# Optimization experiments

Hardware: AMD Instinct MI355X
Metric: run time of the kernel (lower is better)

## Reference

```python
import jax, jax.numpy as jnp
import numpy as np

N_NODES = 50000
N_EDGES = 800000
N_GRAPHS = 256
IN_DIM = 128
HID = 512            # hidden_layer_size
H2 = HID // 2        # 256, conv channels
H4 = HID // 4        # 128


def _linear_init(key, fan_in, fan_out):
    kw, kb = jax.random.split(key)
    bound = 1.0 / np.sqrt(fan_in)
    W = jax.random.uniform(kw, (fan_in, fan_out), minval=-bound, maxval=bound, dtype=jnp.float32)
    b = jax.random.uniform(kb, (fan_out,), minval=-bound, maxval=bound, dtype=jnp.float32)
    return W, b


def setup_inputs() -> dict:
    key = jax.random.key(0)
    ks = jax.random.split(key, 8)
    x = jax.random.normal(ks[0], (N_NODES, IN_DIM), dtype=jnp.float32)
    edge_index = jax.random.randint(ks[1], (2, N_EDGES), 0, N_NODES, dtype=jnp.int64)
    batch = jnp.sort(jax.random.randint(ks[2], (N_NODES,), 0, N_GRAPHS, dtype=jnp.int64))
    W1, b1 = _linear_init(ks[3], IN_DIM, HID)
    Wc1, bc1 = _linear_init(ks[4], HID, H2)
    Wc2, bc2 = _linear_init(ks[5], H2, H2)
    W2, b2 = _linear_init(ks[6], H2, H4)
    W3, b3 = _linear_init(ks[7], H4, 1)
    return {"x": x, "edge_index": edge_index, "batch": batch,
            "W1": W1, "b1": b1, "Wc1": Wc1, "bc1": bc1,
            "Wc2": Wc2, "bc2": bc2, "W2": W2, "b2": b2, "W3": W3, "b3": b3}


def _gcn_conv(h, W, b, src, dst, norm):
    # PyG GCNConv: out = scatter_add(norm * (h @ W)[src] -> dst) + b
    hw = h @ W                                   # [N, C_out]
    msg = norm[:, None] * hw[src]                # [E+N, C_out] gather
    agg = jax.ops.segment_sum(msg, dst, num_segments=N_NODES)  # scatter-add
    return agg + b


def reference(x, edge_index, batch, W1, b1, Wc1, bc1, Wc2, bc2, W2, b2, W3, b3):
    # --- symmetric GCN normalization with self-loops (shared by both convs) ---
    loop = jnp.arange(N_NODES, dtype=edge_index.dtype)
    src = jnp.concatenate([edge_index[0], loop])
    dst = jnp.concatenate([edge_index[1], loop])
    deg = jax.ops.segment_sum(jnp.ones_like(dst, dtype=jnp.float32), dst, num_segments=N_NODES)
    dinv = jax.lax.rsqrt(deg)                    # deg >= 1 thanks to self-loops
    norm = dinv[src] * dinv[dst]                 # [E+N]

    h = jax.nn.relu(x @ W1 + b1)                 # lin1
    h = jax.nn.relu(_gcn_conv(h, Wc1, bc1, src, dst, norm))   # conv1
    h = jax.nn.relu(_gcn_conv(h, Wc2, bc2, src, dst, norm))   # conv2

    # global_mean_pool over graph ids
    sums = jax.ops.segment_sum(h, batch, num_segments=N_GRAPHS)
    counts = jax.ops.segment_sum(jnp.ones((N_NODES,), jnp.float32), batch, num_segments=N_GRAPHS)
    g = sums / jnp.maximum(counts, 1.0)[:, None]

    # F.dropout is identity in deterministic/eval reference
    g = jax.nn.relu(g @ W2 + b2)                 # lin2
    return g @ W3 + b3                           # lin3 -> [N_GRAPHS, 1]
```

## Files before the change

kernel.cpp:

```cpp
#include <hip/hip_runtime.h>
#include <hip/hip_bf16.h>

#define NN 50000
#define NE 800000
#define NG 256
#define DIN 128
#define DH 512
#define DC 256
#define DL 128
#define NB 49

#define XBF_OFF   0UL
#define H1BF_OFF  12800000UL
#define HWBF_OFF  64000000UL
#define H2BF_OFF  89600000UL
#define H3BF_OFF  115200000UL
#define W1T_OFF   140800000UL
#define WC1T_OFF  140931072UL
#define WC2T_OFF  141193216UL
#define CNT_OFF   141324288UL
#define FILL_OFF  141524288UL
#define DINV_OFF  141724288UL
#define RP_OFF    141924288UL
#define BSUM_OFF  142124416UL
#define EW_OFF    142124800UL

using bf16x8 = __attribute__((ext_vector_type(8))) short;
using f32x4  = __attribute__((ext_vector_type(4))) float;

__device__ __forceinline__ short f2bf(float f) {
  unsigned u = __builtin_bit_cast(unsigned, f);
  unsigned r = u + 0x7fffu + ((u >> 16) & 1u);
  return (short)(r >> 16);
}
__device__ __forceinline__ float bf2f(unsigned short u) {
  return __builtin_bit_cast(float, (unsigned)u << 16);
}

__device__ __forceinline__ void gload_lds16(const void* g, void* l) {
  typedef const __attribute__((address_space(1))) unsigned gu32;
  typedef __attribute__((address_space(3))) unsigned lu32;
  __builtin_amdgcn_global_load_lds((gu32*)g, (lu32*)l, 16, 0, 0);
}

__global__ void count_in(const int* __restrict__ dst, int* __restrict__ cnt) {
  int e = blockIdx.x * blockDim.x + threadIdx.x;
  if (e < NE) atomicAdd(&cnt[dst[e]], 1);
}

__global__ __launch_bounds__(1024) void scan_p1(const int* __restrict__ cnt,
                                                int* __restrict__ rowptr,
                                                int* __restrict__ bsum,
                                                float* __restrict__ dinv) {
  __shared__ int wsum[16];
  const int idx = blockIdx.x * 1024 + threadIdx.x;
  const int lane = threadIdx.x & 63, wid = threadIdx.x >> 6;
  int v = (idx < NN) ? cnt[idx] : 0;
  int incl = v;
  #pragma unroll
  for (int s = 1; s < 64; s <<= 1) {
    int t = __shfl_up(incl, s, 64);
    if (lane >= s) incl += t;
  }
  if (lane == 63) wsum[wid] = incl;
  __syncthreads();
  if (wid == 0 && lane < 16) {
    int w = wsum[lane];
    int wincl = w;
    #pragma unroll
    for (int s = 1; s < 16; s <<= 1) {
      int t = __shfl_up(wincl, s, 64);
      if (lane >= s) wincl += t;
    }
    wsum[lane] = wincl - w;
    if (lane == 15) bsum[blockIdx.x] = wincl;
  }
  __syncthreads();
  if (idx < NN) {
    rowptr[idx] = wsum[wid] + incl - v;
    dinv[idx] = 1.0f / sqrtf((float)(v + 1));
  }
}

__global__ __launch_bounds__(1024) void scan_p3(int* __restrict__ rowptr,
                                                const int* __restrict__ bsum) {
  __shared__ int off_s;
  const int t = threadIdx.x;
  if (t < 64) {
    int v = (t < NB && t < blockIdx.x) ? bsum[t] : 0;
    #pragma unroll
    for (int s = 32; s > 0; s >>= 1) v += __shfl_down(v, s, 64);
    if (t == 0) off_s = v;
  }
  __syncthreads();
  const int idx = blockIdx.x * 1024 + t;
  if (idx < NN) rowptr[idx] += off_s;
  if (blockIdx.x == 0 && t == 0) rowptr[NN] = NE;
}

__global__ void fill_prep(const int* __restrict__ src, const int* __restrict__ dst,
                          const int* __restrict__ rowptr, int* __restrict__ fill,
                          const float* __restrict__ dinv, unsigned* __restrict__ ewp,
                          const float* __restrict__ x, short* __restrict__ xbf,
                          const float* __restrict__ W1, short* __restrict__ W1t,
                          const float* __restrict__ Wc1, short* __restrict__ Wc1t,
                          const float* __restrict__ Wc2, short* __restrict__ Wc2t) {
  int gidx = blockIdx.x * 256 + threadIdx.x;
  if (gidx < NE) {
    int d = dst[gidx];
    int s = src[gidx];
    int pos = rowptr[d] + atomicAdd(&fill[d], 1);
    float w = dinv[d] * dinv[s];
    ewp[pos] = (unsigned)s | ((unsigned)(unsigned short)f2bf(w) << 16);
    return;
  }
  int idx = gidx - NE;
  if (idx < 800000) {
    const float4* p = (const float4*)x + (long)idx * 2;
    float4 a = p[0], b = p[1];
    bf16x8 o;
    o[0] = f2bf(a.x); o[1] = f2bf(a.y); o[2] = f2bf(a.z); o[3] = f2bf(a.w);
    o[4] = f2bf(b.x); o[5] = f2bf(b.y); o[6] = f2bf(b.z); o[7] = f2bf(b.w);
    *(bf16x8*)(xbf + (long)idx * 8) = o;
  } else if (idx < 865536) {
    int j = idx - 800000;
    int n = j >> 7, k = j & 127;
    W1t[j] = f2bf(W1[k * DH + n]);
  } else if (idx < 996608) {
    int j = idx - 865536;
    int n = j >> 9, k = j & 511;
    Wc1t[j] = f2bf(Wc1[k * DC + n]);
  } else if (idx < 1062144) {
    int j = idx - 996608;
    int n = j >> 8, k = j & 255;
    Wc2t[j] = f2bf(Wc2[k * DC + n]);
  }
}

template<int DO_RELU, int HAS_BIAS>
__global__ __launch_bounds__(256) void gemm_mfma4(
    const short* __restrict__ A,
    const short* __restrict__ Bt,
    const float* __restrict__ bias,
    short* __restrict__ Cout, int M, int K, int N)
{
  __shared__ __align__(16) short As[128][64];
  __shared__ __align__(16) short Bs[128][64];
  const int tid  = threadIdx.x;
  const int lane = tid & 63;
  const int wave = tid >> 6;
  const int wr   = wave >> 1;
  const int wc   = wave & 1;
  const int bm = blockIdx.y * 128;
  const int bn = blockIdx.x * 128;

  const int srow = lane >> 3;
  const int scol = (lane & 7) * 8;

  f32x4 acc[4][4];
  #pragma unroll
  for (int m = 0; m < 4; ++m)
    #pragma unroll
    for (int n = 0; n < 4; ++n)
      acc[m][n] = f32x4{0.f, 0.f, 0.f, 0.f};

  const int fr = lane & 15;
  const int kb = (lane >> 4) * 8;

  for (int k0 = 0; k0 < K; k0 += 64) {
    #pragma unroll
    for (int j = 0; j < 4; ++j) {
      const int r = wave * 32 + j * 8;
      gload_lds16(A  + (long)(bm + r + srow) * K + k0 + scol, &As[r][0]);
      gload_lds16(Bt + (long)(bn + r + srow) * K + k0 + scol, &Bs[r][0]);
    }
    __syncthreads();
    #pragma unroll
    for (int kk = 0; kk < 2; ++kk) {
      bf16x8 af[4], bfr[4];
      #pragma unroll
      for (int m = 0; m < 4; ++m)
        af[m] = *(const bf16x8*)&As[wr * 64 + m * 16 + fr][kk * 32 + kb];
      #pragma unroll
      for (int n = 0; n < 4; ++n)
        bfr[n] = *(const bf16x8*)&Bs[wc * 64 + n * 16 + fr][kk * 32 + kb];
      #pragma unroll
      for (int m = 0; m < 4; ++m)
        #pragma unroll
        for (int n = 0; n < 4; ++n)
          acc[m][n] = __builtin_amdgcn_mfma_f32_16x16x32_bf16(af[m], bfr[n], acc[m][n], 0, 0, 0);
    }
    __syncthreads();
  }

  const int cr4 = (lane >> 4) * 4;
  const int cc  = lane & 15;
  #pragma unroll
  for (int m = 0; m < 4; ++m) {
    #pragma unroll
    for (int r = 0; r < 4; ++r) {
      int gm = bm + wr * 64 + m * 16 + cr4 + r;
      if (gm >= M) continue;
      #pragma unroll
      for (int n = 0; n < 4; ++n) {
        int gn = bn + wc * 64 + n * 16 + cc;
        float v = acc[m][n][r];
        if (HAS_BIAS) v += bias[gn];
        if (DO_RELU) v = fmaxf(v, 0.f);
        Cout[(long)gm * N + gn] = f2bf(v);
      }
    }
  }
}

__global__ __launch_bounds__(256) void aggregate_v6(
    const unsigned short* __restrict__ hw, const unsigned* __restrict__ ewp,
    const int* __restrict__ rowptr, const float* __restrict__ dinv,
    const float* __restrict__ bias, unsigned short* __restrict__ out)
{
  const int wid  = threadIdx.x >> 6;
  const int lane = threadIdx.x & 63;
  const int i = blockIdx.x * 4 + wid;
  if (i >= NN) return;
  const int c0 = lane * 4;
  const float di = dinv[i];

  ushort4 sv = *(const ushort4*)(hw + (long)i * DC + c0);
  const float dii = di * di;
  float acc0 = dii * bf2f(sv.x);
  float acc1 = dii * bf2f(sv.y);
  float acc2 = dii * bf2f(sv.z);
  float acc3 = dii * bf2f(sv.w);

  const int s0 = rowptr[i], s1 = rowptr[i + 1];
  int e = s0;
  for (; e + 8 <= s1; e += 8) {
    unsigned pk[8]; ushort4 vv[8];
    #pragma unroll
    for (int j = 0; j < 8; ++j) pk[j] = __builtin_nontemporal_load(ewp + e + j);
    #pragma unroll
    for (int j = 0; j < 8; ++j)
      vv[j] = *(const ushort4*)(hw + (long)(pk[j] & 0xffffu) * DC + c0);
    #pragma unroll
    for (int j = 0; j < 8; ++j) {
      float w = bf2f((unsigned short)(pk[j] >> 16));
      acc0 += w * bf2f(vv[j].x);
      acc1 += w * bf2f(vv[j].y);
      acc2 += w * bf2f(vv[j].z);
      acc3 += w * bf2f(vv[j].w);
    }
  }
  for (; e + 4 <= s1; e += 4) {
    unsigned pk[4]; ushort4 vv[4];
    #pragma unroll
    for (int j = 0; j < 4; ++j) pk[j] = __builtin_nontemporal_load(ewp + e + j);
    #pragma unroll
    for (int j = 0; j < 4; ++j)
      vv[j] = *(const ushort4*)(hw + (long)(pk[j] & 0xffffu) * DC + c0);
    #pragma unroll
    for (int j = 0; j < 4; ++j) {
      float w = bf2f((unsigned short)(pk[j] >> 16));
      acc0 += w * bf2f(vv[j].x);
      acc1 += w * bf2f(vv[j].y);
      acc2 += w * bf2f(vv[j].z);
      acc3 += w * bf2f(vv[j].w);
    }
  }
  for (; e < s1; ++e) {
    unsigned pk = __builtin_nontemporal_load(ewp + e);
    float w = bf2f((unsigned short)(pk >> 16));
    ushort4 v = *(const ushort4*)(hw + (long)(pk & 0xffffu) * DC + c0);
    acc0 += w * bf2f(v.x);
    acc1 += w * bf2f(v.y);
    acc2 += w * bf2f(v.z);
    acc3 += w * bf2f(v.w);
  }
  const float4 bv = *(const float4*)(bias + c0);
  ushort4 o;
  o.x = (unsigned short)f2bf(fmaxf(acc0 + bv.x, 0.f));
  o.y = (unsigned short)f2bf(fmaxf(acc1 + bv.y, 0.f));
  o.z = (unsigned short)f2bf(fmaxf(acc2 + bv.z, 0.f));
  o.w = (unsigned short)f2bf(fmaxf(acc3 + bv.w, 0.f));
  unsigned long long po = __builtin_bit_cast(unsigned long long, o);
  __builtin_nontemporal_store(po, (unsigned long long*)(out + (long)i * DC + c0));
}

__global__ __launch_bounds__(256) void pool_mlp_v3(
    const unsigned short* __restrict__ h, const int* __restrict__ batch,
    const float* __restrict__ W2, const float* __restrict__ b2,
    const float* __restrict__ W3, const float* __restrict__ b3,
    float* __restrict__ out)
{
  __shared__ float part[4][DC];
  __shared__ float gmean[DC];
  __shared__ float red[DL];
  const int g = blockIdx.x;
  const int t = threadIdx.x;
  const int wid = t >> 6;
  const int lane = t & 63;
  const int c0 = lane * 4;

  int lo = 0, hi = NN;
  while (lo < hi) { int mid = (lo + hi) >> 1; if (batch[mid] < g) lo = mid + 1; else hi = mid; }
  const int start = lo;
  hi = NN;
  while (lo < hi) { int mid = (lo + hi) >> 1; if (batch[mid] < g + 1) lo = mid + 1; else hi = mid; }
  const int end = lo;

  float4 a0 = {0.f, 0.f, 0.f, 0.f}, a1 = {0.f, 0.f, 0.f, 0.f};
  int i = start + wid;
  for (; i + 4 < end; i += 8) {
    ushort4 v0 = *(const ushort4*)(h + (long)i * DC + c0);
    ushort4 v1 = *(const ushort4*)(h + (long)(i + 4) * DC + c0);
    a0.x += bf2f(v0.x); a0.y += bf2f(v0.y); a0.z += bf2f(v0.z); a0.w += bf2f(v0.w);
    a1.x += bf2f(v1.x); a1.y += bf2f(v1.y); a1.z += bf2f(v1.z); a1.w += bf2f(v1.w);
  }
  if (i < end) {
    ushort4 v0 = *(const ushort4*)(h + (long)i * DC + c0);
    a0.x += bf2f(v0.x); a0.y += bf2f(v0.y); a0.z += bf2f(v0.z); a0.w += bf2f(v0.w);
  }
  a0.x += a1.x; a0.y += a1.y; a0.z += a1.z; a0.w += a1.w;
  *(float4*)&part[wid][c0] = a0;
  __syncthreads();
  if (wid == 0) {
    const float inv = 1.0f / fmaxf((float)(end - start), 1.f);
    float4 s0 = *(const float4*)&part[0][c0];
    float4 s1 = *(const float4*)&part[1][c0];
    float4 s2 = *(const float4*)&part[2][c0];
    float4 s3 = *(const float4*)&part[3][c0];
    float4 m;
    m.x = (s0.x + s1.x + s2.x + s3.x) * inv;
    m.y = (s0.y + s1.y + s2.y + s3.y) * inv;
    m.z = (s0.z + s1.z + s2.z + s3.z) * inv;
    m.w = (s0.w + s1.w + s2.w + s3.w) * inv;
    *(float4*)&gmean[c0] = m;
  }
  __syncthreads();
  if (t < DL) {
    float acc = b2[t];
    for (int k = 0; k < DC; ++k) acc = fmaf(gmean[k], W2[k * DL + t], acc);
    red[t] = fmaxf(acc, 0.f) * W3[t];
  }
  __syncthreads();
  for (int s2 = 64; s2 > 0; s2 >>= 1) {
    if (t < s2) red[t] += red[t + s2];
    __syncthreads();
  }
  if (t == 0) out[g] = red[0] + b3[0];
}

extern "C" void kernel_launch(void* const* d_in, const int* in_sizes, int n_in,
                              void* d_out, int out_size, void* d_ws, size_t ws_size,
                              hipStream_t stream) {
  const float* x    = (const float*)d_in[0];
  const int*   ei   = (const int*)d_in[1];
  const int*   bat  = (const int*)d_in[2];
  const float* W1   = (const float*)d_in[3];
  const float* b1   = (const float*)d_in[4];
  const float* Wc1  = (const float*)d_in[5];
  const float* bc1  = (const float*)d_in[6];
  const float* Wc2  = (const float*)d_in[7];
  const float* bc2  = (const float*)d_in[8];
  const float* W2   = (const float*)d_in[9];
  const float* b2   = (const float*)d_in[10];
  const float* W3   = (const float*)d_in[11];
  const float* b3   = (const float*)d_in[12];
  float* out = (float*)d_out;

  char* ws = (char*)d_ws;
  short* xbf    = (short*)(ws + XBF_OFF);
  short* h1bf   = (short*)(ws + H1BF_OFF);
  unsigned short* hwbf = (unsigned short*)(ws + HWBF_OFF);
  unsigned short* h2bf = (unsigned short*)(ws + H2BF_OFF);
  unsigned short* h3bf = (unsigned short*)(ws + H3BF_OFF);
  short* W1t    = (short*)(ws + W1T_OFF);
  short* Wc1t   = (short*)(ws + WC1T_OFF);
  short* Wc2t   = (short*)(ws + WC2T_OFF);
  int*   cnt    = (int*)  (ws + CNT_OFF);
  int*   fill   = (int*)  (ws + FILL_OFF);
  float* dinv   = (float*)(ws + DINV_OFF);
  int*   rowptr = (int*)  (ws + RP_OFF);
  int*   bsum   = (int*)  (ws + BSUM_OFF);
  unsigned* ewp = (unsigned*)(ws + EW_OFF);

  const int* srcE = ei;
  const int* dstE = ei + NE;

  hipMemsetAsync(cnt, 0, 2 * NN * sizeof(int), stream);

  count_in<<<(NE + 255) / 256, 256, 0, stream>>>(dstE, cnt);
  scan_p1<<<NB, 1024, 0, stream>>>(cnt, rowptr, bsum, dinv);
  scan_p3<<<NB, 1024, 0, stream>>>(rowptr, bsum);
  fill_prep<<<(NE + 1062144 + 255) / 256, 256, 0, stream>>>(
      srcE, dstE, rowptr, fill, dinv, ewp,
      x, xbf, W1, W1t, Wc1, Wc1t, Wc2, Wc2t);

  {
    dim3 grid(DH / 128, (NN + 127) / 128);
    gemm_mfma4<1, 1><<<grid, 256, 0, stream>>>(xbf, W1t, b1, h1bf, NN, DIN, DH);
  }
  {
    dim3 grid(DC / 128, (NN + 127) / 128);
    gemm_mfma4<0, 0><<<grid, 256, 0, stream>>>(h1bf, Wc1t, nullptr, (short*)hwbf, NN, DH, DC);
  }
  aggregate_v6<<<(NN + 3) / 4, 256, 0, stream>>>(hwbf, ewp, rowptr, dinv, bc1, h2bf);
  {
    dim3 grid(DC / 128, (NN + 127) / 128);
    gemm_mfma4<0, 0><<<grid, 256, 0, stream>>>((const short*)h2bf, Wc2t, nullptr, (short*)hwbf, NN, DC, DC);
  }
  aggregate_v6<<<(NN + 3) / 4, 256, 0, stream>>>(hwbf, ewp, rowptr, dinv, bc2, h3bf);

  pool_mlp_v3<<<NG, 256, 0, stream>>>(h3bf, bat, W2, b2, W3, b3, out);
}
```

Measured before the change: 321.4 us.

## Fold CSR scan stages into GEMM launches and swizzle LDS tiles

Moves edge-degree counting into the dtype-conversion prep kernel. The two scan phases now run as extra 256-thread blocks that share a launch with the lin1 and conv1 GEMMs, and CSR fill moves after those GEMMs, which cuts the number of serial kernel launches. The GEMM's LDS tile gets an XOR swizzle on 16-byte column chunks to reduce bank conflicts on the MFMA fragment reads. The GEMMs now use 1D grids with explicit block-index decoding. The scan shrinks to 196 blocks of 256 threads. Scan blocks and GEMM blocks in the same grid use different amounts of work and LDS, which may unbalance the launch.

New measurement: 306.2 us. 4.8% less time.

```diff
diff --git a/kernel.cpp b/kernel.cpp
--- a/kernel.cpp
+++ b/kernel.cpp
@@ -8,7 +8,7 @@
 #define DH 512
 #define DC 256
 #define DL 128
-#define NB 49
+#define NSB 196
 
 #define XBF_OFF   0UL
 #define H1BF_OFF  12800000UL
@@ -23,7 +23,7 @@
 #define DINV_OFF  141724288UL
 #define RP_OFF    141924288UL
 #define BSUM_OFF  142124416UL
-#define EW_OFF    142124800UL
+#define EW_OFF    142125440UL
 
 using bf16x8 = __attribute__((ext_vector_type(8))) short;
 using f32x4  = __attribute__((ext_vector_type(4))) float;
@@ -43,17 +43,46 @@
   __builtin_amdgcn_global_load_lds((gu32*)g, (lu32*)l, 16, 0, 0);
 }
 
-__global__ void count_in(const int* __restrict__ dst, int* __restrict__ cnt) {
-  int e = blockIdx.x * blockDim.x + threadIdx.x;
-  if (e < NE) atomicAdd(&cnt[dst[e]], 1);
-}
-
-__global__ __launch_bounds__(1024) void scan_p1(const int* __restrict__ cnt,
-                                                int* __restrict__ rowptr,
-                                                int* __restrict__ bsum,
-                                                float* __restrict__ dinv) {
-  __shared__ int wsum[16];
-  const int idx = blockIdx.x * 1024 + threadIdx.x;
+__global__ __launch_bounds__(256) void prep0(
+    const int* __restrict__ src, const int* __restrict__ dst, int* __restrict__ cnt,
+    const float* __restrict__ x, short* __restrict__ xbf,
+    const float* __restrict__ W1, short* __restrict__ W1t,
+    const float* __restrict__ Wc1, short* __restrict__ Wc1t,
+    const float* __restrict__ Wc2, short* __restrict__ Wc2t) {
+  long gidx = (long)blockIdx.x * 256 + threadIdx.x;
+  if (gidx < NE) {
+    atomicAdd(&cnt[dst[gidx]], 1);
+    return;
+  }
+  long idx = gidx - NE;
+  if (idx < 800000) {
+    const float4* p = (const float4*)x + idx * 2;
+    float4 a = p[0], b = p[1];
+    bf16x8 o;
+    o[0] = f2bf(a.x); o[1] = f2bf(a.y); o[2] = f2bf(a.z); o[3] = f2bf(a.w);
+    o[4] = f2bf(b.x); o[5] = f2bf(b.y); o[6] = f2bf(b.z); o[7] = f2bf(b.w);
+    *(bf16x8*)(xbf + idx * 8) = o;
+  } else if (idx < 865536) {
+    int j = (int)(idx - 800000);
+    int n = j >> 7, k = j & 127;
+    W1t[j] = f2bf(W1[k * DH + n]);
+  } else if (idx < 996608) {
+    int j = (int)(idx - 865536);
+    int n = j >> 9, k = j & 511;
+    Wc1t[j] = f2bf(Wc1[k * DC + n]);
+  } else if (idx < 1062144) {
+    int j = (int)(idx - 996608);
+    int n = j >> 8, k = j & 255;
+    Wc2t[j] = f2bf(Wc2[k * DC + n]);
+  }
+}
+
+__device__ __forceinline__ void scan_p1_body(
+    const int* __restrict__ cnt, int* __restrict__ rowptr,
+    int* __restrict__ bsum, float* __restrict__ dinv) {
+  __shared__ int wsum[4];
+  const int b = blockIdx.x;
+  const int idx = b * 256 + threadIdx.x;
   const int lane = threadIdx.x & 63, wid = threadIdx.x >> 6;
   int v = (idx < NN) ? cnt[idx] : 0;
   int incl = v;
@@ -64,85 +93,50 @@
   }
   if (lane == 63) wsum[wid] = incl;
   __syncthreads();
-  if (wid == 0 && lane < 16) {
-    int w = wsum[lane];
-    int wincl = w;
-    #pragma unroll
-    for (int s = 1; s < 16; s <<= 1) {
-      int t = __shfl_up(wincl, s, 64);
-      if (lane >= s) wincl += t;
-    }
-    wsum[lane] = wincl - w;
-    if (lane == 15) bsum[blockIdx.x] = wincl;
-  }
+  int woff = 0;
+  for (int w = 0; w < wid; ++w) woff += wsum[w];
+  if (idx < NN) {
+    rowptr[idx] = woff + incl - v;
+    dinv[idx] = 1.0f / sqrtf((float)(v + 1));
+  }
+  if (threadIdx.x == 255) bsum[b] = woff + incl;
+}
+
+__device__ __forceinline__ void scan_p3_body(
+    int* __restrict__ rowptr, const int* __restrict__ bsum) {
+  __shared__ int r4[4];
+  const int b = blockIdx.x;
+  const int t = threadIdx.x;
+  const int lane = t & 63, wid = t >> 6;
+  int v = (t < b) ? bsum[t] : 0;
+  #pragma unroll
+  for (int s = 32; s > 0; s >>= 1) v += __shfl_down(v, s, 64);
+  if (lane == 0) r4[wid] = v;
   __syncthreads();
-  if (idx < NN) {
-    rowptr[idx] = wsum[wid] + incl - v;
-    dinv[idx] = 1.0f / sqrtf((float)(v + 1));
-  }
-}
-
-__global__ __launch_bounds__(1024) void scan_p3(int* __restrict__ rowptr,
-                                                const int* __restrict__ bsum) {
-  __shared__ int off_s;
-  const int t = threadIdx.x;
-  if (t < 64) {
-    int v = (t < NB && t < blockIdx.x) ? bsum[t] : 0;
-    #pragma unroll
-    for (int s = 32; s > 0; s >>= 1) v += __shfl_down(v, s, 64);
-    if (t == 0) off_s = v;
-  }
-  __syncthreads();
-  const int idx = blockIdx.x * 1024 + t;
-  if (idx < NN) rowptr[idx] += off_s;
-  if (blockIdx.x == 0 && t == 0) rowptr[NN] = NE;
-}
-
-__global__ void fill_prep(const int* __restrict__ src, const int* __restrict__ dst,
-                          const int* __restrict__ rowptr, int* __restrict__ fill,
-                          const float* __restrict__ dinv, unsigned* __restrict__ ewp,
-                          const float* __restrict__ x, short* __restrict__ xbf,
-                          const float* __restrict__ W1, short* __restrict__ W1t,
-                          const float* __restrict__ Wc1, short* __restrict__ Wc1t,
-                          const float* __restrict__ Wc2, short* __restrict__ Wc2t) {
-  int gidx = blockIdx.x * 256 + threadIdx.x;
-  if (gidx < NE) {
-    int d = dst[gidx];
-    int s = src[gidx];
+  const int off = r4[0] + r4[1] + r4[2] + r4[3];
+  const int idx = b * 256 + t;
+  if (idx < NN) rowptr[idx] += off;
+  if (b == 0 && t == 0) rowptr[NN] = NE;
+}
+
+__global__ void fill_csr(const int* __restrict__ src, const int* __restrict__ dst,
+                         const int* __restrict__ rowptr, int* __restrict__ fill,
+                         const float* __restrict__ dinv, unsigned* __restrict__ ewp) {
+  int e = blockIdx.x * blockDim.x + threadIdx.x;
+  if (e < NE) {
+    int d = dst[e];
+    int s = src[e];
     int pos = rowptr[d] + atomicAdd(&fill[d], 1);
     float w = dinv[d] * dinv[s];
     ewp[pos] = (unsigned)s | ((unsigned)(unsigned short)f2bf(w) << 16);
-    return;
-  }
-  int idx = gidx - NE;
-  if (idx < 800000) {
-    const float4* p = (const float4*)x + (long)idx * 2;
-    float4 a = p[0], b = p[1];
-    bf16x8 o;
-    o[0] = f2bf(a.x); o[1] = f2bf(a.y); o[2] = f2bf(a.z); o[3] = f2bf(a.w);
-    o[4] = f2bf(b.x); o[5] = f2bf(b.y); o[6] = f2bf(b.z); o[7] = f2bf(b.w);
-    *(bf16x8*)(xbf + (long)idx * 8) = o;
-  } else if (idx < 865536) {
-    int j = idx - 800000;
-    int n = j >> 7, k = j & 127;
-    W1t[j] = f2bf(W1[k * DH + n]);
-  } else if (idx < 996608) {
-    int j = idx - 865536;
-    int n = j >> 9, k = j & 511;
-    Wc1t[j] = f2bf(Wc1[k * DC + n]);
-  } else if (idx < 1062144) {
-    int j = idx - 996608;
-    int n = j >> 8, k = j & 255;
-    Wc2t[j] = f2bf(Wc2[k * DC + n]);
   }
 }
 
 template<int DO_RELU, int HAS_BIAS>
-__global__ __launch_bounds__(256) void gemm_mfma4(
-    const short* __restrict__ A,
-    const short* __restrict__ Bt,
-    const float* __restrict__ bias,
-    short* __restrict__ Cout, int M, int K, int N)
+__device__ __forceinline__ void gemm_body(
+    const short* __restrict__ A, const short* __restrict__ Bt,
+    const float* __restrict__ bias, short* __restrict__ Cout,
+    int M, int K, int N, int bxi, int byi)
 {
   __shared__ __align__(16) short As[128][64];
   __shared__ __align__(16) short Bs[128][64];
@@ -151,11 +145,11 @@
   const int wave = tid >> 6;
   const int wr   = wave >> 1;
   const int wc   = wave & 1;
-  const int bm = blockIdx.y * 128;
-  const int bn = blockIdx.x * 128;
+  const int bm = byi * 128;
+  const int bn = bxi * 128;
 
   const int srow = lane >> 3;
-  const int scol = (lane & 7) * 8;
+  const int scol = ((lane & 7) ^ srow) * 8;
 
   f32x4 acc[4][4];
   #pragma unroll
@@ -164,8 +158,9 @@
     for (int n = 0; n < 4; ++n)
       acc[m][n] = f32x4{0.f, 0.f, 0.f, 0.f};
 
-  const int fr = lane & 15;
-  const int kb = (lane >> 4) * 8;
+  const int fr  = lane & 15;
+  const int g4  = lane >> 4;
+  const int frx = fr & 7;
 
   for (int k0 = 0; k0 < K; k0 += 64) {
     #pragma unroll
@@ -177,13 +172,14 @@
     __syncthreads();
     #pragma unroll
     for (int kk = 0; kk < 2; ++kk) {
+      const int col = ((kk * 4 + g4) ^ frx) * 8;
       bf16x8 af[4], bfr[4];
       #pragma unroll
       for (int m = 0; m < 4; ++m)
-        af[m] = *(const bf16x8*)&As[wr * 64 + m * 16 + fr][kk * 32 + kb];
+        af[m] = *(const bf16x8*)&As[wr * 64 + m * 16 + fr][col];
       #pragma unroll
       for (int n = 0; n < 4; ++n)
-        bfr[n] = *(const bf16x8*)&Bs[wc * 64 + n * 16 + fr][kk * 32 + kb];
+        bfr[n] = *(const bf16x8*)&Bs[wc * 64 + n * 16 + fr][col];
       #pragma unroll
       for (int m = 0; m < 4; ++m)
         #pragma unroll
@@ -211,6 +207,34 @@
       }
     }
   }
+}
+
+__global__ __launch_bounds__(256) void gemm_lin1(
+    const short* __restrict__ A, const short* __restrict__ Bt,
+    const float* __restrict__ bias, short* __restrict__ Cout,
+    const int* __restrict__ cnt, int* __restrict__ rowptr,
+    int* __restrict__ bsum, float* __restrict__ dinv)
+{
+  if (blockIdx.x < NSB) { scan_p1_body(cnt, rowptr, bsum, dinv); return; }
+  int gb = blockIdx.x - NSB;
+  gemm_body<1, 1>(A, Bt, bias, Cout, NN, DIN, DH, gb & 3, gb >> 2);
+}
+
+__global__ __launch_bounds__(256) void gemm_conv1(
+    const short* __restrict__ A, const short* __restrict__ Bt,
+    short* __restrict__ Cout, int* __restrict__ rowptr,
+    const int* __restrict__ bsum)
+{
+  if (blockIdx.x < NSB) { scan_p3_body(rowptr, bsum); return; }
+  int gb = blockIdx.x - NSB;
+  gemm_body<0, 0>(A, Bt, nullptr, Cout, NN, DH, DC, gb & 1, gb >> 1);
+}
+
+__global__ __launch_bounds__(256) void gemm_conv2(
+    const short* __restrict__ A, const short* __restrict__ Bt,
+    short* __restrict__ Cout)
+{
+  gemm_body<0, 0>(A, Bt, nullptr, Cout, NN, DC, DC, blockIdx.x & 1, blockIdx.x >> 1);
 }
 
 __global__ __launch_bounds__(256) void aggregate_v6(
@@ -388,26 +412,17 @@
 
   hipMemsetAsync(cnt, 0, 2 * NN * sizeof(int), stream);
 
-  count_in<<<(NE + 255) / 256, 256, 0, stream>>>(dstE, cnt);
-  scan_p1<<<NB, 1024, 0, stream>>>(cnt, rowptr, bsum, dinv);
-  scan_p3<<<NB, 1024, 0, stream>>>(rowptr, bsum);
-  fill_prep<<<(NE + 1062144 + 255) / 256, 256, 0, stream>>>(
-      srcE, dstE, rowptr, fill, dinv, ewp,
-      x, xbf, W1, W1t, Wc1, Wc1t, Wc2, Wc2t);
-
-  {
-    dim3 grid(DH / 128, (NN + 127) / 128);
-    gemm_mfma4<1, 1><<<grid, 256, 0, stream>>>(xbf, W1t, b1, h1bf, NN, DIN, DH);
-  }
-  {
-    dim3 grid(DC / 128, (NN + 127) / 128);
-    gemm_mfma4<0, 0><<<grid, 256, 0, stream>>>(h1bf, Wc1t, nullptr, (short*)hwbf, NN, DH, DC);
-  }
+  prep0<<<(NE + 1062144 + 255) / 256, 256, 0, stream>>>(
+      srcE, dstE, cnt, x, xbf, W1, W1t, Wc1, Wc1t, Wc2, Wc2t);
+
+  gemm_lin1<<<NSB + 4 * 391, 256, 0, stream>>>(xbf, W1t, b1, h1bf,
+                                               cnt, rowptr, bsum, dinv);
+  gemm_conv1<<<NSB + 2 * 391, 256, 0, stream>>>(h1bf, Wc1t, (short*)hwbf,
+                                                rowptr, bsum);
+  fill_csr<<<(NE + 255) / 256, 256, 0, stream>>>(srcE, dstE, rowptr, fill, dinv, ewp);
+
   aggregate_v6<<<(NN + 3) / 4, 256, 0, stream>>>(hwbf, ewp, rowptr, dinv, bc1, h2bf);
-  {
-    dim3 grid(DC / 128, (NN + 127) / 128);
-    gemm_mfma4<0, 0><<<grid, 256, 0, stream>>>((const short*)h2bf, Wc2t, nullptr, (short*)hwbf, NN, DC, DC);
-  }
+  gemm_conv2<<<2 * 391, 256, 0, stream>>>((const short*)h2bf, Wc2t, (short*)hwbf);
   aggregate_v6<<<(NN + 3) / 4, 256, 0, stream>>>(hwbf, ewp, rowptr, dinv, bc2, h3bf);
 
   pool_mlp_v3<<<NG, 256, 0, stream>>>(h3bf, bat, W2, b2, W3, b3, out);
```
